# Kernel tuning notes

Measured on AMD Instinct MI355X. Metric: run time of the kernel, lower is better.

## Reference

```python
import jax, jax.numpy as jnp
import numpy as np

B, N, CIN, H, OUT, L, K = 8, 512, 64, 64, 64, 256, 3
EPS = 1e-5


def setup_inputs() -> dict:
    key = jax.random.key(0)
    ks = jax.random.split(key, 12)
    def unif(k, shape, fan):
        s = 1.0 / np.sqrt(fan)
        return jax.random.uniform(k, shape, jnp.float32, -s, s)
    return {
        "x": jax.random.normal(ks[0], (B, N, CIN, L), jnp.float32),
        "adj": jax.random.uniform(ks[1], (B, N, N), jnp.float32),
        # temp_conv1: Conv1d(CIN->H, k=3)
        "w1": unif(ks[2], (H, CIN, K), CIN * K),
        "b1": unif(ks[3], (H,), CIN * K),
        # graph_conv: Linear-style (H,H) + bias, stdv=1/sqrt(out_features)
        "gw": unif(ks[4], (H, H), H),
        "gb": unif(ks[5], (H,), H),
        # temp_conv2: Conv1d(H->OUT, k=3)
        "w2": unif(ks[6], (OUT, H, K), H * K),
        "b2": unif(ks[7], (OUT,), H * K),
        # residual: Conv1d(CIN->OUT, k=1) == pointwise linear
        "wr": unif(ks[8], (OUT, CIN), CIN),
        "br": unif(ks[9], (OUT,), CIN),
        # BatchNorm2d(OUT) affine params
        "gamma": jnp.ones((OUT,), jnp.float32),
        "beta": jnp.zeros((OUT,), jnp.float32),
    }


def _conv1d(x, w, b, pad):
    # x: (B, N, C, L) -> flatten node dim into batch, NCH conv
    b_, n_, c, l = x.shape
    y = jax.lax.conv_general_dilated(
        x.reshape(b_ * n_, c, l), w, window_strides=(1,),
        padding=[(pad, pad)], dimension_numbers=("NCH", "OIH", "NCH"))
    y = y + b[None, :, None]
    return y.reshape(b_, n_, w.shape[0], l)


def reference(x, adj, w1, b1, gw, gb, w2, b2, wr, br, gamma, beta):
    pad = (K - 1) // 2
    # residual branch: 1x1 conv over channels
    residual = jnp.einsum("bncl,oc->bnol", x, wr) + br[None, None, :, None]
    # temporal conv 1
    out = _conv1d(x, w1, b1, pad)                      # (B,N,H,L)
    # graph conv over all timesteps at once (replaces per-t Python loop)
    xw = jnp.einsum("bnhl,hd->bndl", out, gw)          # (B,N,H,L)
    out = jnp.einsum("bnm,bmdl->bndl", adj, xw) + gb[None, None, :, None]
    # temporal conv 2
    out = _conv1d(out, w2, b2, pad)                    # (B,N,OUT,L)
    out = out + residual
    # BatchNorm2d over channel axis (training-mode batch stats, biased var)
    mean = jnp.mean(out, axis=(0, 1, 3), keepdims=True)
    var = jnp.mean(jnp.square(out - mean), axis=(0, 1, 3), keepdims=True)
    out = (out - mean) * jax.lax.rsqrt(var + EPS)
    out = out * gamma[None, None, :, None] + beta[None, None, :, None]
    return jax.nn.relu(out)
```

## Files before the change

kernel.cpp:

```cpp
#include <hip/hip_runtime.h>
#include <hip/hip_bf16.h>
#include <stdint.h>


typedef unsigned short u16;
typedef unsigned int   u32;
typedef __attribute__((ext_vector_type(8))) short           bf16x8;
typedef __attribute__((ext_vector_type(8))) unsigned short  u16x8;
typedef __attribute__((ext_vector_type(4))) unsigned short  u16x4;
typedef __attribute__((ext_vector_type(4))) float           f32x4;

__device__ __forceinline__ float bf2f(u16 v){
  union { u32 u; float f; } x; x.u = ((u32)v) << 16; return x.f;
}
__device__ __forceinline__ u16 f2bf(float f){
  __hip_bfloat16 h = __float2bfloat16(f);
  return *reinterpret_cast<u16*>(&h);
}
__device__ __forceinline__ u32 swz(int row, int cbyte){
  return (u32)(row * 128) + (u32)(cbyte ^ ((row & 7) << 4));
}

__global__ __launch_bounds__(256) void k_prep(const float* __restrict__ w1, const float* __restrict__ b1,
    const float* __restrict__ gw, const float* __restrict__ w2, const float* __restrict__ wr,
    u16* __restrict__ w1g, float* __restrict__ b1g, u16* __restrict__ w2t, u16* __restrict__ wrt){
  const int gt = blockIdx.x * 256 + threadIdx.x, gs = gridDim.x * 256;
  for (int e = gt; e < 12288; e += gs){
    int tap = e >> 12, rem = e & 4095, o = rem >> 6, c = rem & 63;
    w2t[e] = f2bf(w2[(o * 64 + c) * 3 + tap]);
    float s = 0.f;
    for (int h = 0; h < 64; ++h)
      s += gw[h * 64 + o] * w1[(h * 64 + c) * 3 + tap];
    w1g[e] = f2bf(s);
  }
  for (int e = gt; e < 4096; e += gs) wrt[e] = f2bf(wr[e]);
  for (int d = gt; d < 64; d += gs){
    float s = 0.f;
    for (int h = 0; h < 64; ++h) s += b1[h] * gw[h * 64 + d];
    b1g[d] = s;
  }
}

__global__ __launch_bounds__(256) void k_p1(const float* __restrict__ x,
    const u16* __restrict__ w1g, const float* __restrict__ b1g,
    const u16* __restrict__ wrt, u16* __restrict__ outA, u16* __restrict__ outR){
  __shared__ u16 tile[16384];
  const int t = threadIdx.x;
  const size_t bn = (size_t)blockIdx.x + (size_t)blockIdx.y * 512;
  const float* xb = x + bn * 16384;

  {
    const int c0 = (t >> 3) * 2;
    #pragma unroll
    for (int v = 0; v < 8; ++v){
      const int l0 = (t & 7) * 4 + v * 32;
      f32x4 a = *(const f32x4*)(xb + (size_t)c0 * 256 + l0);
      f32x4 b = *(const f32x4*)(xb + (size_t)(c0 + 1) * 256 + l0);
      #pragma unroll
      for (int e = 0; e < 4; ++e){
        u32 p = (u32)f2bf(a[e]) | ((u32)f2bf(b[e]) << 16);
        *(u32*)((char*)tile + swz(l0 + e, c0 * 2)) = p;
      }
    }
  }
  __syncthreads();
  const int w = t >> 6, ln = t & 63, lq = ln >> 4, lr = ln & 15;
  const bf16x8 z8 = {};

  {
    f32x4 racc[4][4];
    #pragma unroll
    for (int i = 0; i < 4; ++i)
      #pragma unroll
      for (int j = 0; j < 4; ++j) racc[i][j] = (f32x4){0.f, 0.f, 0.f, 0.f};
    #pragma unroll
    for (int kk = 0; kk < 2; ++kk){
      bf16x8 A[4];
      #pragma unroll
      for (int fo = 0; fo < 4; ++fo)
        A[fo] = *(const bf16x8*)(wrt + (fo * 16 + lr) * 64 + kk * 32 + lq * 8);
      #pragma unroll
      for (int fc = 0; fc < 4; ++fc){
        int l = w * 64 + fc * 16 + lr;
        bf16x8 B = *(const bf16x8*)((char*)tile + swz(l, kk * 64 + lq * 16));
        #pragma unroll
        for (int fo = 0; fo < 4; ++fo)
          racc[fo][fc] = __builtin_amdgcn_mfma_f32_16x16x32_bf16(A[fo], B, racc[fo][fc], 0, 0, 0);
      }
    }
    u16* rp = outR + bn * 16384 + t * 64;
    #pragma unroll
    for (int v = 0; v < 8; ++v){
      u16x8 ov;
      const int fo = v >> 1;
      #pragma unroll
      for (int h = 0; h < 2; ++h){
        const int fc = (v & 1) * 2 + h;
        #pragma unroll
        for (int r2 = 0; r2 < 4; ++r2)
          ov[h * 4 + r2] = f2bf(racc[fo][fc][r2]);
      }
      *(u16x8*)(rp + v * 8) = ov;
    }
  }

  f32x4 acc[4][4];
  #pragma unroll
  for (int i = 0; i < 4; ++i)
    #pragma unroll
    for (int j = 0; j < 4; ++j) acc[i][j] = (f32x4){0.f, 0.f, 0.f, 0.f};
  #pragma unroll
  for (int tap = 0; tap < 3; ++tap){
    #pragma unroll
    for (int kk = 0; kk < 2; ++kk){
      bf16x8 A[4];
      #pragma unroll
      for (int fo = 0; fo < 4; ++fo)
        A[fo] = *(const bf16x8*)(w1g + tap * 4096 + (fo * 16 + lr) * 64 + kk * 32 + lq * 8);
      #pragma unroll
      for (int fc = 0; fc < 4; ++fc){
        int r = w * 64 + fc * 16 + lr + tap - 1;
        int rc = r < 0 ? 0 : (r > 255 ? 255 : r);
        bf16x8 B = *(const bf16x8*)((char*)tile + swz(rc, kk * 64 + lq * 16));
        if (r != rc) B = z8;
        #pragma unroll
        for (int fo = 0; fo < 4; ++fo)
          acc[fo][fc] = __builtin_amdgcn_mfma_f32_16x16x32_bf16(A[fo], B, acc[fo][fc], 0, 0, 0);
      }
    }
  }
  __syncthreads();
  #pragma unroll
  for (int fo = 0; fo < 4; ++fo){
    float bb[4];
    #pragma unroll
    for (int r2 = 0; r2 < 4; ++r2) bb[r2] = b1g[fo * 16 + lq * 4 + r2];
    #pragma unroll
    for (int fc = 0; fc < 4; ++fc){
      int l = w * 64 + fc * 16 + lr;
      #pragma unroll
      for (int r2 = 0; r2 < 4; ++r2){
        int d = fo * 16 + lq * 4 + r2;
        *(u16*)((char*)tile + l * 128 + ((2 * d) ^ ((l & 7) << 4))) = f2bf(acc[fo][fc][r2] + bb[r2]);
      }
    }
  }
  __syncthreads();
  u16* op = outA + bn * 16384;
  #pragma unroll
  for (int v = 0; v < 8; ++v){
    int flat = v * 2048 + t * 8;
    int l = flat >> 6, d0 = flat & 63;
    u16x8 val = *(const u16x8*)((char*)tile + l * 128 + ((d0 * 2) ^ ((l & 7) << 4)));
    *(u16x8*)(op + flat) = val;
  }
}

__global__ __launch_bounds__(256) void k_p3(const u16* __restrict__ xw,
    const float* __restrict__ adj, const float* __restrict__ gbv, u16* __restrict__ outB){
  __shared__ u16 At[8192];
  __shared__ u16 Bt[8192];
  const int t = threadIdx.x;
  const int wg = ((blockIdx.x & 7) << 9) | ((int)blockIdx.x >> 3);
  const int jt = wg & 127, nt = (wg >> 7) & 3, b = wg >> 9;
  const float* adjb = adj + ((size_t)b * 512 + (size_t)nt * 128) * 512;
  const u16* Xb = xw + (size_t)b * 8388608 + (size_t)jt * 128;
  const int w = t >> 6, ln = t & 63, lq = ln >> 4, lr = ln & 15;
  const int wrow = w >> 1, wcol = w & 1;
  const int mpair = t & 31, jq = t >> 5;
  f32x4 acc[4][4];
  #pragma unroll
  for (int i = 0; i < 4; ++i)
    #pragma unroll
    for (int j = 0; j < 4; ++j) acc[i][j] = (f32x4){0.f, 0.f, 0.f, 0.f};

  f32x4 ra[8];
  u16x8 rb[4];
  auto LOADK = [&](int ks){
    #pragma unroll
    for (int it = 0; it < 8; ++it){
      int c = it * 256 + t;
      int row = c >> 4, mc = c & 15;
      ra[it] = *(const f32x4*)(adjb + (size_t)row * 512 + ks * 64 + mc * 4);
    }
    const u16* s0 = Xb + (size_t)(ks * 64 + mpair * 2) * 16384 + jq * 16;
    const u16* s1 = s0 + 16384;
    #pragma unroll
    for (int v2 = 0; v2 < 2; ++v2){
      rb[v2 * 2]     = *(const u16x8*)(s0 + v2 * 8);
      rb[v2 * 2 + 1] = *(const u16x8*)(s1 + v2 * 8);
    }
  };

  LOADK(0);
  for (int ks = 0; ks < 8; ++ks){
    #pragma unroll
    for (int it = 0; it < 8; ++it){
      int c = it * 256 + t;
      int row = c >> 4, mc = c & 15;
      u16x4 pk;
      #pragma unroll
      for (int e = 0; e < 4; ++e) pk[e] = f2bf(ra[it][e]);
      *(u16x4*)((char*)At + (u32)(row * 128) + (u32)((mc * 8) ^ ((row & 7) << 4))) = pk;
    }
    #pragma unroll
    for (int v2 = 0; v2 < 2; ++v2){
      #pragma unroll
      for (int e = 0; e < 8; ++e){
        u32 p = (u32)(u16)rb[v2 * 2][e] | ((u32)(u16)rb[v2 * 2 + 1][e] << 16);
        *(u32*)((char*)Bt + swz(jq * 16 + v2 * 8 + e, mpair * 4)) = p;
      }
    }
    __syncthreads();
    if (ks < 7) LOADK(ks + 1);
    #pragma unroll
    for (int kk = 0; kk < 2; ++kk){
      bf16x8 Af[4], Bf[4];
      #pragma unroll
      for (int f = 0; f < 4; ++f){
        int rA = wrow * 64 + f * 16 + lr;
        Af[f] = *(const bf16x8*)((char*)At + swz(rA, kk * 64 + lq * 16));
        int rB = wcol * 64 + f * 16 + lr;
        Bf[f] = *(const bf16x8*)((char*)Bt + swz(rB, kk * 64 + lq * 16));
      }
      #pragma unroll
      for (int fr = 0; fr < 4; ++fr)
        #pragma unroll
        for (int fc = 0; fc < 4; ++fc)
          acc[fr][fc] = __builtin_amdgcn_mfma_f32_16x16x32_bf16(Af[fr], Bf[fc], acc[fr][fc], 0, 0, 0);
    }
    __syncthreads();
  }
  float gbl[4];
  #pragma unroll
  for (int fc = 0; fc < 4; ++fc) gbl[fc] = gbv[fc * 16 + lr];
  u16* ob = outB + ((size_t)b * 512 + (size_t)nt * 128) * 16384 + (size_t)jt * 128;
  #pragma unroll
  for (int fr = 0; fr < 4; ++fr)
    #pragma unroll
    for (int fc = 0; fc < 4; ++fc)
      #pragma unroll
      for (int r2 = 0; r2 < 4; ++r2){
        int n_ = wrow * 64 + fr * 16 + lq * 4 + r2;
        int j_ = wcol * 64 + fc * 16 + lr;
        ob[(size_t)n_ * 16384 + j_] = f2bf(acc[fr][fc][r2] + gbl[fc]);
      }
}

__global__ __launch_bounds__(256) void k_p4(const u16* __restrict__ g,
    const u16* __restrict__ resv, const u16* __restrict__ w2t,
    const float* __restrict__ b2v, const float* __restrict__ brv,
    u16* __restrict__ outP, float* __restrict__ spart){
  __shared__ u16 gt2[16384];
  __shared__ float sc2[512];
  const int t = threadIdx.x;
  const size_t bn = (size_t)blockIdx.x + (size_t)blockIdx.y * 512;
  const u16* gb = g + bn * 16384;
  #pragma unroll
  for (int v = 0; v < 8; ++v){
    int flat = v * 2048 + t * 8;
    int l = flat >> 6, d0 = flat & 63;
    u16x8 val = *(const u16x8*)(gb + flat);
    *(u16x8*)((char*)gt2 + l * 128 + ((d0 * 2) ^ ((l & 7) << 4))) = val;
  }
  __syncthreads();
  const int w = t >> 6, ln = t & 63, lq = ln >> 4, lr = ln & 15;
  const bf16x8 z8 = {};

  const u16* rp = resv + bn * 16384 + t * 64;
  u16x8 rv[8];
  #pragma unroll
  for (int v = 0; v < 8; ++v) rv[v] = *(const u16x8*)(rp + v * 8);

  f32x4 acc[4][4];
  #pragma unroll
  for (int i = 0; i < 4; ++i)
    #pragma unroll
    for (int j = 0; j < 4; ++j) acc[i][j] = (f32x4){0.f, 0.f, 0.f, 0.f};

  #pragma unroll
  for (int tap = 0; tap < 3; ++tap){
    #pragma unroll
    for (int kk = 0; kk < 2; ++kk){
      bf16x8 A[4];
      #pragma unroll
      for (int fo = 0; fo < 4; ++fo)
        A[fo] = *(const bf16x8*)(w2t + tap * 4096 + (fo * 16 + lr) * 64 + kk * 32 + lq * 8);
      #pragma unroll
      for (int fc = 0; fc < 4; ++fc){
        int r = w * 64 + fc * 16 + lr + tap - 1;
        int rc = r < 0 ? 0 : (r > 255 ? 255 : r);
        bf16x8 B = *(const bf16x8*)((char*)gt2 + swz(rc, kk * 64 + lq * 16));
        if (r != rc) B = z8;
        #pragma unroll
        for (int fo = 0; fo < 4; ++fo)
          acc[fo][fc] = __builtin_amdgcn_mfma_f32_16x16x32_bf16(A[fo], B, acc[fo][fc], 0, 0, 0);
      }
    }
  }
  __syncthreads();

  float psum[16], psq[16];
  #pragma unroll
  for (int i = 0; i < 16; ++i){ psum[i] = 0.f; psq[i] = 0.f; }
  #pragma unroll
  for (int fo = 0; fo < 4; ++fo){
    float bb[4];
    #pragma unroll
    for (int r2 = 0; r2 < 4; ++r2){
      int o = fo * 16 + lq * 4 + r2;
      bb[r2] = b2v[o] + brv[o];
    }
    #pragma unroll
    for (int fc = 0; fc < 4; ++fc){
      int l = w * 64 + fc * 16 + lr;
      #pragma unroll
      for (int r2 = 0; r2 < 4; ++r2){
        float val = acc[fo][fc][r2] + bb[r2]
                  + bf2f(rv[fo * 2 + (fc >> 1)][(fc & 1) * 4 + r2]);
        int o = fo * 16 + lq * 4 + r2;
        gt2[o * 256 + (l ^ ((o & 7) * 8))] = f2bf(val);
        psum[fo * 4 + r2] += val;
        psq[fo * 4 + r2] += val * val;
      }
    }
  }
  #pragma unroll
  for (int i = 0; i < 16; ++i){
    #pragma unroll
    for (int m = 1; m < 16; m <<= 1){
      psum[i] += __shfl_xor(psum[i], m, 64);
      psq[i]  += __shfl_xor(psq[i],  m, 64);
    }
  }
  if (lr == 0){
    #pragma unroll
    for (int i = 0; i < 16; ++i){
      int o = (i >> 2) * 16 + lq * 4 + (i & 3);
      sc2[w * 128 + o]      = psum[i];
      sc2[w * 128 + 64 + o] = psq[i];
    }
  }
  __syncthreads();
  u16* op = outP + bn * 16384;
  #pragma unroll
  for (int v = 0; v < 8; ++v){
    int d = (t >> 5) + v * 8;
    int l0 = (t & 31) * 8;
    u16x8 val = *(const u16x8*)(gt2 + d * 256 + (l0 ^ ((d & 7) * 8)));
    *(u16x8*)(op + v * 2048 + t * 8) = val;
  }
  if (t < 128){
    float tot = sc2[t] + sc2[128 + t] + sc2[256 + t] + sc2[384 + t];
    spart[(size_t)t * 4096 + bn] = tot;
  }
}

__global__ __launch_bounds__(256) void k_p5(const float* __restrict__ part, float* __restrict__ fin){
  const int o = blockIdx.x, t = threadIdx.x;
  float s1 = 0.f, s2 = 0.f;
  for (int k = t; k < 4096; k += 256){
    s1 += part[(size_t)o * 4096 + k];
    s2 += part[(size_t)(64 + o) * 4096 + k];
  }
  #pragma unroll
  for (int m = 32; m; m >>= 1){
    s1 += __shfl_down(s1, m, 64);
    s2 += __shfl_down(s2, m, 64);
  }
  __shared__ float red[8];
  if ((t & 63) == 0){ red[(t >> 6) * 2] = s1; red[(t >> 6) * 2 + 1] = s2; }
  __syncthreads();
  if (t == 0){
    float S1 = red[0] + red[2] + red[4] + red[6];
    float S2 = red[1] + red[3] + red[5] + red[7];
    const float invN = 1.f / 1048576.f;
    float mean = S1 * invN;
    float var = S2 * invN - mean * mean;
    fin[o] = mean;
    fin[64 + o] = rsqrtf(var + 1e-5f);
  }
}

__global__ __launch_bounds__(256) void k_p6(const u16* __restrict__ pre, const float* __restrict__ fin,
    const float* __restrict__ gamma, const float* __restrict__ beta, float* __restrict__ out){
  __shared__ float ssca[64], soff[64];
  const int tt = threadIdx.x;
  if (tt < 64){
    float sc = fin[64 + tt] * gamma[tt];
    ssca[tt] = sc;
    soff[tt] = beta[tt] - fin[tt] * sc;
  }
  __syncthreads();
  const size_t nchunk = 8388608;
  for (size_t i = (size_t)blockIdx.x * 256 + tt; i < nchunk; i += (size_t)gridDim.x * 256){
    int o = (int)((i >> 5) & 63);
    float sca = ssca[o], off = soff[o];
    u16x8 v = *(const u16x8*)(pre + i * 8);
    f32x4 oa, ob;
    #pragma unroll
    for (int e = 0; e < 4; ++e){
      float f0 = bf2f(v[e]) * sca + off;
      float f1 = bf2f(v[4 + e]) * sca + off;
      oa[e] = f0 > 0.f ? f0 : 0.f;
      ob[e] = f1 > 0.f ? f1 : 0.f;
    }
    *(f32x4*)(out + i * 8)     = oa;
    *(f32x4*)(out + i * 8 + 4) = ob;
  }
}

extern "C" void kernel_launch(void* const* d_in, const int* in_sizes, int n_in,
                              void* d_out, int out_size, void* d_ws, size_t ws_size,
                              hipStream_t stream){
  const float* x     = (const float*)d_in[0];
  const float* adj   = (const float*)d_in[1];
  const float* w1    = (const float*)d_in[2];
  const float* b1    = (const float*)d_in[3];
  const float* gw    = (const float*)d_in[4];
  const float* gb    = (const float*)d_in[5];
  const float* w2    = (const float*)d_in[6];
  const float* b2    = (const float*)d_in[7];
  const float* wr    = (const float*)d_in[8];
  const float* br    = (const float*)d_in[9];
  const float* gamma = (const float*)d_in[10];
  const float* beta  = (const float*)d_in[11];
  (void)in_sizes; (void)n_in; (void)out_size; (void)ws_size;

  char* ws = (char*)d_ws;
  u16*   bufA  = (u16*)ws;
  float* spart = (float*)(ws + 134217728);
  float* sfin  = (float*)(ws + 136314880);
  u16*   w1g   = (u16*)(ws + 136315392);
  float* b1g   = (float*)(ws + 136339968);
  u16*   w2t   = (u16*)(ws + 136348160);
  u16*   wrt   = (u16*)(ws + 136372736);
  u16*   gbuf  = (u16*)d_out;
  u16*   bufR  = (u16*)d_out + 67108864;

  k_prep<<<16, 256, 0, stream>>>(w1, b1, gw, w2, wr, w1g, b1g, w2t, wrt);
  k_p1<<<dim3(512, 8, 1), 256, 0, stream>>>(x, w1g, b1g, wrt, bufA, bufR);
  k_p3<<<4096, 256, 0, stream>>>(bufA, adj, gb, gbuf);
  k_p4<<<dim3(512, 8, 1), 256, 0, stream>>>(gbuf, bufR, w2t, b2, br, bufA, spart);
  k_p5<<<64, 256, 0, stream>>>(spart, sfin);
  k_p6<<<2048, 256, 0, stream>>>(bufA, sfin, gamma, beta, (float*)d_out);
}
```

Measured before the change: 553.2 us.

## Give each wave a private haloed LDS stripe to drop block barriers in conv kernels

The two temporal-conv kernels now give each wave its own 72-row LDS stripe: its 64 time rows plus a 4-row halo on each side, zero-filled at the sequence edges. The B-operand reads therefore need no clamping or masking, and the block-wide __syncthreads between load, MFMA and writeback are removed. The residual tensor is written and read in a new, matching layout, and the output stores now follow each wave's own stripe. The cost is redundant halo loads and larger LDS use per block. The x loads in k_p1 are also less coalesced, since each lane reads from a different channel row.

```diff
diff --git a/kernel.cpp b/kernel.cpp
--- a/kernel.cpp
+++ b/kernel.cpp
@@ -7,7 +7,6 @@
 typedef unsigned int   u32;
 typedef __attribute__((ext_vector_type(8))) short           bf16x8;
 typedef __attribute__((ext_vector_type(8))) unsigned short  u16x8;
-typedef __attribute__((ext_vector_type(4))) unsigned short  u16x4;
 typedef __attribute__((ext_vector_type(4))) float           f32x4;
 
 __device__ __forceinline__ float bf2f(u16 v){
@@ -17,8 +16,8 @@
   __hip_bfloat16 h = __float2bfloat16(f);
   return *reinterpret_cast<u16*>(&h);
 }
-__device__ __forceinline__ u32 swz(int row, int cbyte){
-  return (u32)(row * 128) + (u32)(cbyte ^ ((row & 7) << 4));
+__device__ __forceinline__ u32 swzl(int rr, int cb){
+  return (u32)(rr * 128) + (u32)(cb ^ ((rr & 7) << 4));
 }
 
 __global__ __launch_bounds__(256) void k_prep(const float* __restrict__ w1, const float* __restrict__ b1,
@@ -44,28 +43,33 @@
 __global__ __launch_bounds__(256) void k_p1(const float* __restrict__ x,
     const u16* __restrict__ w1g, const float* __restrict__ b1g,
     const u16* __restrict__ wrt, u16* __restrict__ outA, u16* __restrict__ outR){
-  __shared__ u16 tile[16384];
+  __shared__ u16 stripes[18432];
   const int t = threadIdx.x;
   const size_t bn = (size_t)blockIdx.x + (size_t)blockIdx.y * 512;
   const float* xb = x + bn * 16384;
+  const int w = t >> 6, ln = t & 63, lq = ln >> 4, lr = ln & 15;
+  char* wbase = (char*)stripes + w * 9216;
 
   {
-    const int c0 = (t >> 3) * 2;
-    #pragma unroll
-    for (int v = 0; v < 8; ++v){
-      const int l0 = (t & 7) * 4 + v * 32;
-      f32x4 a = *(const f32x4*)(xb + (size_t)c0 * 256 + l0);
-      f32x4 b = *(const f32x4*)(xb + (size_t)(c0 + 1) * 256 + l0);
+    const int cp = ln & 31, c0 = cp * 2, cbyte = cp * 4;
+    const int half = ln >> 5;
+    #pragma unroll
+    for (int k = 0; k < 9; ++k){
+      const int rr0 = half * 36 + k * 4;
+      const int g0 = w * 64 - 4 + rr0;
+      const bool oob = (g0 < 0) || (g0 > 252);
+      f32x4 a = {0.f,0.f,0.f,0.f}, b = {0.f,0.f,0.f,0.f};
+      if (!oob){
+        a = *(const f32x4*)(xb + (size_t)c0 * 256 + g0);
+        b = *(const f32x4*)(xb + (size_t)(c0 + 1) * 256 + g0);
+      }
       #pragma unroll
       for (int e = 0; e < 4; ++e){
-        u32 p = (u32)f2bf(a[e]) | ((u32)f2bf(b[e]) << 16);
-        *(u32*)((char*)tile + swz(l0 + e, c0 * 2)) = p;
-      }
-    }
-  }
-  __syncthreads();
-  const int w = t >> 6, ln = t & 63, lq = ln >> 4, lr = ln & 15;
-  const bf16x8 z8 = {};
+        u32 p = oob ? 0u : ((u32)f2bf(a[e]) | ((u32)f2bf(b[e]) << 16));
+        *(u32*)(wbase + swzl(rr0 + e, cbyte)) = p;
+      }
+    }
+  }
 
   {
     f32x4 racc[4][4];
@@ -81,14 +85,12 @@
         A[fo] = *(const bf16x8*)(wrt + (fo * 16 + lr) * 64 + kk * 32 + lq * 8);
       #pragma unroll
       for (int fc = 0; fc < 4; ++fc){
-        int l = w * 64 + fc * 16 + lr;
-        bf16x8 B = *(const bf16x8*)((char*)tile + swz(l, kk * 64 + lq * 16));
+        bf16x8 B = *(const bf16x8*)(wbase + swzl(fc * 16 + lr + 4, kk * 64 + lq * 16));
         #pragma unroll
         for (int fo = 0; fo < 4; ++fo)
           racc[fo][fc] = __builtin_amdgcn_mfma_f32_16x16x32_bf16(A[fo], B, racc[fo][fc], 0, 0, 0);
       }
     }
-    u16* rp = outR + bn * 16384 + t * 64;
     #pragma unroll
     for (int v = 0; v < 8; ++v){
       u16x8 ov;
@@ -100,7 +102,7 @@
         for (int r2 = 0; r2 < 4; ++r2)
           ov[h * 4 + r2] = f2bf(racc[fo][fc][r2]);
       }
-      *(u16x8*)(rp + v * 8) = ov;
+      *(u16x8*)(outR + bn * 16384 + v * 2048 + t * 8) = ov;
     }
   }
 
@@ -119,17 +121,13 @@
         A[fo] = *(const bf16x8*)(w1g + tap * 4096 + (fo * 16 + lr) * 64 + kk * 32 + lq * 8);
       #pragma unroll
       for (int fc = 0; fc < 4; ++fc){
-        int r = w * 64 + fc * 16 + lr + tap - 1;
-        int rc = r < 0 ? 0 : (r > 255 ? 255 : r);
-        bf16x8 B = *(const bf16x8*)((char*)tile + swz(rc, kk * 64 + lq * 16));
-        if (r != rc) B = z8;
+        bf16x8 B = *(const bf16x8*)(wbase + swzl(fc * 16 + lr + tap + 3, kk * 64 + lq * 16));
         #pragma unroll
         for (int fo = 0; fo < 4; ++fo)
           acc[fo][fc] = __builtin_amdgcn_mfma_f32_16x16x32_bf16(A[fo], B, acc[fo][fc], 0, 0, 0);
       }
     }
   }
-  __syncthreads();
   #pragma unroll
   for (int fo = 0; fo < 4; ++fo){
     float bb[4];
@@ -137,22 +135,21 @@
     for (int r2 = 0; r2 < 4; ++r2) bb[r2] = b1g[fo * 16 + lq * 4 + r2];
     #pragma unroll
     for (int fc = 0; fc < 4; ++fc){
-      int l = w * 64 + fc * 16 + lr;
+      const int ll = fc * 16 + lr;
       #pragma unroll
       for (int r2 = 0; r2 < 4; ++r2){
-        int d = fo * 16 + lq * 4 + r2;
-        *(u16*)((char*)tile + l * 128 + ((2 * d) ^ ((l & 7) << 4))) = f2bf(acc[fo][fc][r2] + bb[r2]);
-      }
-    }
-  }
-  __syncthreads();
+        const int d = fo * 16 + lq * 4 + r2;
+        *(u16*)(wbase + ll * 128 + ((2 * d) ^ ((ll & 7) << 4))) = f2bf(acc[fo][fc][r2] + bb[r2]);
+      }
+    }
+  }
   u16* op = outA + bn * 16384;
   #pragma unroll
   for (int v = 0; v < 8; ++v){
-    int flat = v * 2048 + t * 8;
-    int l = flat >> 6, d0 = flat & 63;
-    u16x8 val = *(const u16x8*)((char*)tile + l * 128 + ((d0 * 2) ^ ((l & 7) << 4)));
-    *(u16x8*)(op + flat) = val;
+    const int ll = v * 8 + (ln >> 3);
+    const int d0 = (ln & 7) * 8;
+    u16x8 val = *(const u16x8*)(wbase + ll * 128 + ((d0 * 2) ^ ((ll & 7) << 4)));
+    *(u16x8*)(op + (size_t)(w * 64 + ll) * 64 + d0) = val;
   }
 }
 
@@ -198,17 +195,17 @@
     for (int it = 0; it < 8; ++it){
       int c = it * 256 + t;
       int row = c >> 4, mc = c & 15;
-      u16x4 pk;
+      __attribute__((ext_vector_type(4))) unsigned short pk;
       #pragma unroll
       for (int e = 0; e < 4; ++e) pk[e] = f2bf(ra[it][e]);
-      *(u16x4*)((char*)At + (u32)(row * 128) + (u32)((mc * 8) ^ ((row & 7) << 4))) = pk;
+      *(decltype(pk)*)((char*)At + (u32)(row * 128) + (u32)((mc * 8) ^ ((row & 7) << 4))) = pk;
     }
     #pragma unroll
     for (int v2 = 0; v2 < 2; ++v2){
       #pragma unroll
       for (int e = 0; e < 8; ++e){
         u32 p = (u32)(u16)rb[v2 * 2][e] | ((u32)(u16)rb[v2 * 2 + 1][e] << 16);
-        *(u32*)((char*)Bt + swz(jq * 16 + v2 * 8 + e, mpair * 4)) = p;
+        *(u32*)((char*)Bt + swzl(jq * 16 + v2 * 8 + e, mpair * 4)) = p;
       }
     }
     __syncthreads();
@@ -219,9 +216,9 @@
       #pragma unroll
       for (int f = 0; f < 4; ++f){
         int rA = wrow * 64 + f * 16 + lr;
-        Af[f] = *(const bf16x8*)((char*)At + swz(rA, kk * 64 + lq * 16));
+        Af[f] = *(const bf16x8*)((char*)At + swzl(rA, kk * 64 + lq * 16));
         int rB = wcol * 64 + f * 16 + lr;
-        Bf[f] = *(const bf16x8*)((char*)Bt + swz(rB, kk * 64 + lq * 16));
+        Bf[f] = *(const bf16x8*)((char*)Bt + swzl(rB, kk * 64 + lq * 16));
       }
       #pragma unroll
       for (int fr = 0; fr < 4; ++fr)
@@ -251,26 +248,26 @@
     const u16* __restrict__ resv, const u16* __restrict__ w2t,
     const float* __restrict__ b2v, const float* __restrict__ brv,
     u16* __restrict__ outP, float* __restrict__ spart){
-  __shared__ u16 gt2[16384];
+  __shared__ u16 stripes[18432];
   __shared__ float sc2[512];
   const int t = threadIdx.x;
   const size_t bn = (size_t)blockIdx.x + (size_t)blockIdx.y * 512;
-  const u16* gb = g + bn * 16384;
-  #pragma unroll
-  for (int v = 0; v < 8; ++v){
-    int flat = v * 2048 + t * 8;
-    int l = flat >> 6, d0 = flat & 63;
-    u16x8 val = *(const u16x8*)(gb + flat);
-    *(u16x8*)((char*)gt2 + l * 128 + ((d0 * 2) ^ ((l & 7) << 4))) = val;
-  }
-  __syncthreads();
+  const u16* gbp = g + bn * 16384;
   const int w = t >> 6, ln = t & 63, lq = ln >> 4, lr = ln & 15;
-  const bf16x8 z8 = {};
-
-  const u16* rp = resv + bn * 16384 + t * 64;
+  char* wbase = (char*)stripes + w * 9216;
+
+  #pragma unroll
+  for (int it = 0; it < 9; ++it){
+    const int rr = it * 8 + (ln >> 3);
+    const int gl = w * 64 - 4 + rr;
+    u16x8 val = {};
+    if (gl >= 0 && gl <= 255) val = *(const u16x8*)(gbp + (size_t)gl * 64 + (ln & 7) * 8);
+    *(u16x8*)(wbase + rr * 128 + (((ln & 7) * 16) ^ ((rr & 7) << 4))) = val;
+  }
+
   u16x8 rv[8];
   #pragma unroll
-  for (int v = 0; v < 8; ++v) rv[v] = *(const u16x8*)(rp + v * 8);
+  for (int v = 0; v < 8; ++v) rv[v] = *(const u16x8*)(resv + bn * 16384 + v * 2048 + t * 8);
 
   f32x4 acc[4][4];
   #pragma unroll
@@ -288,17 +285,13 @@
         A[fo] = *(const bf16x8*)(w2t + tap * 4096 + (fo * 16 + lr) * 64 + kk * 32 + lq * 8);
       #pragma unroll
       for (int fc = 0; fc < 4; ++fc){
-        int r = w * 64 + fc * 16 + lr + tap - 1;
-        int rc = r < 0 ? 0 : (r > 255 ? 255 : r);
-        bf16x8 B = *(const bf16x8*)((char*)gt2 + swz(rc, kk * 64 + lq * 16));
-        if (r != rc) B = z8;
+        bf16x8 B = *(const bf16x8*)(wbase + swzl(fc * 16 + lr + tap + 3, kk * 64 + lq * 16));
         #pragma unroll
         for (int fo = 0; fo < 4; ++fo)
           acc[fo][fc] = __builtin_amdgcn_mfma_f32_16x16x32_bf16(A[fo], B, acc[fo][fc], 0, 0, 0);
       }
     }
   }
-  __syncthreads();
 
   float psum[16], psq[16];
   #pragma unroll
@@ -313,18 +306,27 @@
     }
     #pragma unroll
     for (int fc = 0; fc < 4; ++fc){
-      int l = w * 64 + fc * 16 + lr;
+      const int ll = fc * 16 + lr;
       #pragma unroll
       for (int r2 = 0; r2 < 4; ++r2){
         float val = acc[fo][fc][r2] + bb[r2]
                   + bf2f(rv[fo * 2 + (fc >> 1)][(fc & 1) * 4 + r2]);
-        int o = fo * 16 + lq * 4 + r2;
-        gt2[o * 256 + (l ^ ((o & 7) * 8))] = f2bf(val);
+        const int o = fo * 16 + lq * 4 + r2;
+        *(u16*)(wbase + o * 128 + ((2 * ll) ^ ((o & 7) << 4))) = f2bf(val);
         psum[fo * 4 + r2] += val;
         psq[fo * 4 + r2] += val * val;
       }
     }
   }
+  u16* op = outP + bn * 16384;
+  #pragma unroll
+  for (int v = 0; v < 8; ++v){
+    const int o = v * 8 + (ln >> 3);
+    const int l0 = (ln & 7) * 8;
+    u16x8 val = *(const u16x8*)(wbase + o * 128 + ((l0 * 2) ^ ((o & 7) << 4)));
+    *(u16x8*)(op + o * 256 + w * 64 + l0) = val;
+  }
+
   #pragma unroll
   for (int i = 0; i < 16; ++i){
     #pragma unroll
@@ -342,14 +344,6 @@
     }
   }
   __syncthreads();
-  u16* op = outP + bn * 16384;
-  #pragma unroll
-  for (int v = 0; v < 8; ++v){
-    int d = (t >> 5) + v * 8;
-    int l0 = (t & 31) * 8;
-    u16x8 val = *(const u16x8*)(gt2 + d * 256 + (l0 ^ ((d & 7) * 8)));
-    *(u16x8*)(op + v * 2048 + t * 8) = val;
-  }
   if (t < 128){
     float tot = sc2[t] + sc2[128 + t] + sc2[256 + t] + sc2[384 + t];
     spart[(size_t)t * 4096 + bn] = tot;
```

Result: slower. 667.8 us (+20.7%).
